# Optimization experiments

Measured on AMD Instinct MI355X. Metric: run time of the kernel, lower is better.

The kernel has to match this reference:

```python
import jax, jax.numpy as jnp
import numpy as np

B, T_OBS, K_PRED, D, U = 1024, 100, 20, 256, 256
T = T_OBS + K_PRED  # len(time_steps) = T_obs + len(time_pred)


def setup_inputs() -> dict:
    key = jax.random.key(0)
    ks = jax.random.split(key, 7)
    latents = jax.random.normal(ks[0], (B, T_OBS, D), dtype=jnp.float32)
    time_steps = jnp.linspace(0.0, 1.0, T, dtype=jnp.float32)
    time_pred = time_steps[-K_PRED:]  # prediction horizon = last K times
    s1 = 1.0 / np.sqrt(D)
    s2 = 1.0 / np.sqrt(U)
    W1 = jax.random.uniform(ks[1], (D, U), jnp.float32, -s1, s1)
    b1 = jax.random.uniform(ks[2], (U,), jnp.float32, -s1, s1)
    W2 = jax.random.uniform(ks[3], (U, U), jnp.float32, -s2, s2)
    b2 = jax.random.uniform(ks[4], (U,), jnp.float32, -s2, s2)
    W3 = jax.random.uniform(ks[5], (U, D), jnp.float32, -s2, s2)
    b3 = jax.random.uniform(ks[6], (D,), jnp.float32, -s2, s2)
    return dict(latents=latents, time_steps=time_steps, time_pred=time_pred,
                W1=W1, b1=b1, W2=W2, b2=b2, W3=W3, b3=b3)


def reference(latents, time_steps, time_pred, W1, b1, W2, b2, W3, b3):
    # ODE-func MLP: latent_dim -> units -> units -> latent_dim (tanh)
    def ode_f(y):
        h = jnp.tanh(y @ W1 + b1)
        h = jnp.tanh(h @ W2 + b2)
        return h @ W3 + b3

    latents_t = jnp.swapaxes(latents, 0, 1)  # [T_obs, B, D]

    # Replicates the original loop semantics exactly: at iteration i the cell
    # integrates from the (prev_t, t_i) left over from iteration i-1 (single
    # Euler step, since every gap < minimum_step = span/50), THEN updates
    # prev_t = t_i, t_i = time_steps[i], and checks membership in time_pred.
    def step(carry, t_next):
        prev_t, t_i, prev_y, j = carry
        yi = prev_y + ode_f(prev_y) * (t_i - prev_t)  # ODECell Euler step
        is_pred = jnp.any(t_next == time_pred)
        j_safe = jnp.clip(j, 0, T_OBS - 1)
        lat_j = jax.lax.dynamic_index_in_dim(latents_t, j_safe, axis=0, keepdims=False)
        prev_y_new = jnp.where(is_pred, yi, lat_j)
        j_new = j + jnp.where(is_pred, 0, 1)
        return (t_i, t_next, prev_y_new, j_new), yi  # Train setting stores yi_ode

    init = (time_steps[0], time_steps[1], latents[:, 0, :], jnp.int32(1))
    _, ys = jax.lax.scan(step, init, time_steps[1:])  # ys: [T-1, B, D]

    new_latents = jnp.concatenate([latents[:, :1, :], jnp.swapaxes(ys, 0, 1)], axis=1)
    return new_latents  # [B, T, D]
```

## Files before the change

### kernel.cpp

```cpp
#include <hip/hip_runtime.h>
#include <hip/hip_bf16.h>

#define NB 1024
#define NTOBS 100
#define NT 120
#define ND 256
#define LAT_BSTRIDE (NTOBS * ND)
#define OUT_BSTRIDE (NT * ND)

#define SEQ_NBLK 64
#define PAR_ROWS 128
#define PAR_BLKS (98 * (NB / PAR_ROWS))

typedef __attribute__((ext_vector_type(8))) short bf16x8;
typedef __attribute__((ext_vector_type(4))) float f32x4;
typedef __attribute__((ext_vector_type(4))) unsigned u32x4;

__device__ __forceinline__ short f2bf(float f) {
    unsigned u = __float_as_uint(f);
    unsigned r = (u + 0x7fffu + ((u >> 16) & 1u)) >> 16;
    return (short)r;
}

__device__ __forceinline__ unsigned cvt_pk_bf16(float lo, float hi) {
    unsigned r;
    asm("v_cvt_pk_bf16_f32 %0, %1, %2" : "=v"(r) : "v"(lo), "v"(hi));
    return r;
}

__device__ __forceinline__ float pade_tanh(float x) {
    float t = fminf(fmaxf(x, -3.0f), 3.0f);
    float t2 = t * t;
    float num = t * (27.0f + t2);
    float den = __builtin_fmaf(9.0f, t2, 27.0f);
    return num * __builtin_amdgcn_rcpf(den);
}

__device__ __forceinline__ int yswz(int r, int c) {
    return (r * 1024 + c * 4) ^ ((r & 7) << 5);
}
__device__ __forceinline__ int aswz(int r, int c) {
    return (r * 512 + c * 2) ^ ((r & 7) << 4);
}

__global__ void prep_kernel(const float* __restrict__ W1,
                            const float* __restrict__ W2,
                            const float* __restrict__ W3,
                            const float* __restrict__ lat,
                            short* __restrict__ wt,
                            float* __restrict__ out)
{
    int tid = blockIdx.x * blockDim.x + threadIdx.x;
    int nth = gridDim.x * blockDim.x;
    for (int i = tid; i < 65536; i += nth) {
        const int j    = i & 7;
        const int lane = (i >> 3) & 63;
        const int kk   = (i >> 9) & 7;
        const int ct16 = i >> 12;
        const int k = kk * 32 + (lane >> 4) * 8 + j;
        const int n = ct16 * 16 + (lane & 15);
        wt[i]              = f2bf(W1[k * 256 + n]);
        wt[i + 65536]      = f2bf(W2[k * 256 + n]);
        wt[i + 2 * 65536]  = f2bf(W3[k * 256 + n]);
    }
    for (int i = tid; i < NB * ND; i += nth) {
        int b = i >> 8, c = i & 255;
        out[(size_t)b * OUT_BSTRIDE + 0 * ND + c] = lat[(size_t)b * LAT_BSTRIDE + 0 * ND + c];
        out[(size_t)b * OUT_BSTRIDE + 2 * ND + c] = lat[(size_t)b * LAT_BSTRIDE + 1 * ND + c];
    }
}

__device__ __forceinline__ void par_layer(f32x4 (&acc)[4][4],
    const char* __restrict__ srcbuf, const short* __restrict__ wtl,
    int rg, int cg, int lane, int l16, int lgr)
{
#pragma unroll
    for (int rt = 0; rt < 4; rt++)
#pragma unroll
        for (int ct = 0; ct < 4; ct++)
            acc[rt][ct] = (f32x4){0.f, 0.f, 0.f, 0.f};

    bf16x8 bpf[4][4];
#pragma unroll
    for (int kk = 0; kk < 4; kk++) {
#pragma unroll
        for (int ct = 0; ct < 4; ct++)
            bpf[kk][ct] = *(const bf16x8*)(wtl + ((cg * 4 + ct) * 8 + kk) * 512 + lane * 8);
    }

#pragma unroll
    for (int kk = 0; kk < 8; kk++) {
        const int k0 = kk * 32 + lgr * 8;
        bf16x8 b[4];
#pragma unroll
        for (int ct = 0; ct < 4; ct++) b[ct] = bpf[kk & 3][ct];
        if (kk < 4) {
#pragma unroll
            for (int ct = 0; ct < 4; ct++)
                bpf[kk][ct] = *(const bf16x8*)(wtl + ((cg * 4 + ct) * 8 + (kk + 4)) * 512 + lane * 8);
        }
        bf16x8 a[4];
#pragma unroll
        for (int rt = 0; rt < 4; rt++) {
            const int r = rg * 64 + rt * 16 + l16;
            a[rt] = *(const bf16x8*)(srcbuf + aswz(r, k0));
        }
#pragma unroll
        for (int rt = 0; rt < 4; rt++)
#pragma unroll
            for (int ct = 0; ct < 4; ct++)
                acc[rt][ct] = __builtin_amdgcn_mfma_f32_16x16x32_bf16(a[rt], b[ct], acc[rt][ct], 0, 0, 0);
    }
}

__device__ __forceinline__ void par_store_h(char* __restrict__ dst,
    const f32x4 (&acc)[4][4], const float bc[4], int rg, int cg, int l16, int lgr)
{
#pragma unroll
    for (int rt = 0; rt < 4; rt++)
#pragma unroll
        for (int ct = 0; ct < 4; ct++) {
            const int c = cg * 64 + ct * 16 + l16;
#pragma unroll
            for (int j = 0; j < 4; j++) {
                const int r = rg * 64 + rt * 16 + lgr * 4 + j;
                *(short*)(dst + aswz(r, c)) = f2bf(pade_tanh(acc[rt][ct][j] + bc[ct]));
            }
        }
}

__global__ __launch_bounds__(512, 2) void ode_main(
    const float* __restrict__ lat, const float* __restrict__ ts,
    const short* __restrict__ wt,
    const float* __restrict__ b1, const float* __restrict__ b2,
    const float* __restrict__ b3, float* __restrict__ out)
{
    __shared__ __align__(16) char smem[131072];

    const int tid = threadIdx.x;
    const int lane = tid & 63, wave = tid >> 6;
    const int l16 = lane & 15, lgr = lane >> 4;
    const short* wt1 = wt;
    const short* wt2 = wt + 65536;
    const short* wt3 = wt + 2 * 65536;

    if (blockIdx.x < SEQ_NBLK) {
        const int b0 = blockIdx.x * 16;
        char* s_y  = smem;
        char* s_h1 = smem + 16384;
        char* s_h2 = smem + 24576;

        bf16x8 w1r[2][8], w2r[2][8], w3r[2][8];
        float bb1[2], bb2[2], bb3[2];
#pragma unroll
        for (int ct = 0; ct < 2; ct++) {
            const int col = wave * 32 + ct * 16 + l16;
            bb1[ct] = b1[col]; bb2[ct] = b2[col]; bb3[ct] = b3[col];
#pragma unroll
            for (int kk = 0; kk < 8; kk++) {
                const int fo = ((wave * 2 + ct) * 8 + kk) * 512 + lane * 8;
                w1r[ct][kk] = *(const bf16x8*)(wt1 + fo);
                w2r[ct][kk] = *(const bf16x8*)(wt2 + fo);
                w3r[ct][kk] = *(const bf16x8*)(wt3 + fo);
            }
        }
        for (int i = tid; i < 16 * 256 / 4; i += 512) {
            const int r = i >> 6, c = (i & 63) * 4;
            f32x4 v = *(const f32x4*)(lat + (size_t)(b0 + r) * LAT_BSTRIDE + 99 * ND + c);
            *(f32x4*)(smem + yswz(r, c)) = v;
        }
        __syncthreads();

#pragma unroll 1
        for (int step = 0; step < 20; step++) {
            const int k = 100 + step;
            const float dt = ts[k - 1] - ts[k - 2];
            f32x4 acc0, acc1;

            acc0 = (f32x4){0.f, 0.f, 0.f, 0.f};
            acc1 = (f32x4){0.f, 0.f, 0.f, 0.f};
#pragma unroll
            for (int kk = 0; kk < 8; kk++) {
                const int k0 = kk * 32 + lgr * 8;
                f32x4 lo = *(const f32x4*)(s_y + yswz(l16, k0));
                f32x4 hi = *(const f32x4*)(s_y + yswz(l16, k0 + 4));
                u32x4 p;
                p[0] = cvt_pk_bf16(lo[0], lo[1]);
                p[1] = cvt_pk_bf16(lo[2], lo[3]);
                p[2] = cvt_pk_bf16(hi[0], hi[1]);
                p[3] = cvt_pk_bf16(hi[2], hi[3]);
                bf16x8 a = *(bf16x8*)&p;
                acc0 = __builtin_amdgcn_mfma_f32_16x16x32_bf16(a, w1r[0][kk], acc0, 0, 0, 0);
                acc1 = __builtin_amdgcn_mfma_f32_16x16x32_bf16(a, w1r[1][kk], acc1, 0, 0, 0);
            }
#pragma unroll
            for (int ct = 0; ct < 2; ct++) {
                const f32x4 av = ct ? acc1 : acc0;
                const int c = wave * 32 + ct * 16 + l16;
#pragma unroll
                for (int j = 0; j < 4; j++) {
                    const int r = lgr * 4 + j;
                    *(short*)(s_h1 + aswz(r, c)) = f2bf(pade_tanh(av[j] + bb1[ct]));
                }
            }
            __syncthreads();

            acc0 = (f32x4){0.f, 0.f, 0.f, 0.f};
            acc1 = (f32x4){0.f, 0.f, 0.f, 0.f};
#pragma unroll
            for (int kk = 0; kk < 8; kk++) {
                const int k0 = kk * 32 + lgr * 8;
                bf16x8 a = *(const bf16x8*)(s_h1 + aswz(l16, k0));
                acc0 = __builtin_amdgcn_mfma_f32_16x16x32_bf16(a, w2r[0][kk], acc0, 0, 0, 0);
                acc1 = __builtin_amdgcn_mfma_f32_16x16x32_bf16(a, w2r[1][kk], acc1, 0, 0, 0);
            }
#pragma unroll
            for (int ct = 0; ct < 2; ct++) {
                const f32x4 av = ct ? acc1 : acc0;
                const int c = wave * 32 + ct * 16 + l16;
#pragma unroll
                for (int j = 0; j < 4; j++) {
                    const int r = lgr * 4 + j;
                    *(short*)(s_h2 + aswz(r, c)) = f2bf(pade_tanh(av[j] + bb2[ct]));
                }
            }
            __syncthreads();

            acc0 = (f32x4){0.f, 0.f, 0.f, 0.f};
            acc1 = (f32x4){0.f, 0.f, 0.f, 0.f};
#pragma unroll
            for (int kk = 0; kk < 8; kk++) {
                const int k0 = kk * 32 + lgr * 8;
                bf16x8 a = *(const bf16x8*)(s_h2 + aswz(l16, k0));
                acc0 = __builtin_amdgcn_mfma_f32_16x16x32_bf16(a, w3r[0][kk], acc0, 0, 0, 0);
                acc1 = __builtin_amdgcn_mfma_f32_16x16x32_bf16(a, w3r[1][kk], acc1, 0, 0, 0);
            }
#pragma unroll
            for (int ct = 0; ct < 2; ct++) {
                const f32x4 av = ct ? acc1 : acc0;
                const int c = wave * 32 + ct * 16 + l16;
                const float bc = ct ? bb3[1] : bb3[0];
#pragma unroll
                for (int j = 0; j < 4; j++) {
                    const int r = lgr * 4 + j;
                    const int yoff = yswz(r, c);
                    const float yold = *(const float*)(s_y + yoff);
                    const float ynew = yold + (av[j] + bc) * dt;
                    *(float*)(s_y + yoff) = ynew;
                    out[(size_t)(b0 + r) * OUT_BSTRIDE + (size_t)k * ND + c] = ynew;
                }
            }
            __syncthreads();
        }
    } else {
        const int p = blockIdx.x - SEQ_NBLK;
        const int e = p >> 3;
        const int b0 = (p & 7) * PAR_ROWS;
        const int src_t = (e == 0) ? 0 : (e + 1);
        const int out_k = (e == 0) ? 1 : (e + 2);
        const float dt = ts[e + 1] - ts[e];
        const float* src = lat + (size_t)b0 * LAT_BSTRIDE + (size_t)src_t * ND;

        char* bufA = smem;
        char* bufH = smem + 65536;
        const int rg = wave >> 2, cg = wave & 3;

#pragma unroll
        for (int t = 0; t < 8; t++) {
            const int i = t * 512 + tid;
            const int r = i >> 5, c0 = (i & 31) * 8;
            const float* pp = src + (size_t)r * LAT_BSTRIDE + c0;
            f32x4 lo = *(const f32x4*)(pp);
            f32x4 hi = *(const f32x4*)(pp + 4);
            u32x4 pk;
            pk[0] = cvt_pk_bf16(lo[0], lo[1]);
            pk[1] = cvt_pk_bf16(lo[2], lo[3]);
            pk[2] = cvt_pk_bf16(hi[0], hi[1]);
            pk[3] = cvt_pk_bf16(hi[2], hi[3]);
            *(u32x4*)(bufA + aswz(r, c0)) = pk;
        }
        __syncthreads();

        f32x4 acc[4][4];
        float bc[4];

#pragma unroll
        for (int ct = 0; ct < 4; ct++) bc[ct] = b1[cg * 64 + ct * 16 + l16];
        par_layer(acc, bufA, wt1, rg, cg, lane, l16, lgr);
        par_store_h(bufH, acc, bc, rg, cg, l16, lgr);
        __syncthreads();

#pragma unroll
        for (int ct = 0; ct < 4; ct++) bc[ct] = b2[cg * 64 + ct * 16 + l16];
        par_layer(acc, bufH, wt2, rg, cg, lane, l16, lgr);
        par_store_h(bufA, acc, bc, rg, cg, l16, lgr);
        __syncthreads();

#pragma unroll
        for (int ct = 0; ct < 4; ct++) bc[ct] = b3[cg * 64 + ct * 16 + l16];
        par_layer(acc, bufA, wt3, rg, cg, lane, l16, lgr);
#pragma unroll
        for (int rt = 0; rt < 4; rt++)
#pragma unroll
            for (int ct = 0; ct < 4; ct++) {
                const int c = cg * 64 + ct * 16 + l16;
#pragma unroll
                for (int j = 0; j < 4; j++) {
                    const int r = rg * 64 + rt * 16 + lgr * 4 + j;
                    const float yold = src[(size_t)r * LAT_BSTRIDE + c];
                    out[(size_t)(b0 + r) * OUT_BSTRIDE + (size_t)out_k * ND + c] =
                        yold + (acc[rt][ct][j] + bc[ct]) * dt;
                }
            }
    }
}

extern "C" void kernel_launch(void* const* d_in, const int* in_sizes, int n_in,
                              void* d_out, int out_size, void* d_ws, size_t ws_size,
                              hipStream_t stream)
{
    const float* lat = (const float*)d_in[0];
    const float* ts  = (const float*)d_in[1];
    const float* W1  = (const float*)d_in[3];
    const float* b1  = (const float*)d_in[4];
    const float* W2  = (const float*)d_in[5];
    const float* b2  = (const float*)d_in[6];
    const float* W3  = (const float*)d_in[7];
    const float* b3  = (const float*)d_in[8];
    float* out = (float*)d_out;
    short* wt = (short*)d_ws;

    hipLaunchKernelGGL(prep_kernel, dim3(256), dim3(256), 0, stream,
                       W1, W2, W3, lat, wt, out);
    hipLaunchKernelGGL(ode_main, dim3(SEQ_NBLK + PAR_BLKS), dim3(512), 0, stream,
                       lat, ts, wt, b1, b2, b3, out);
}
```

Measured before the change: 126.4 us.

## Make parallel MLP blocks persistent with async prefetch of next latent tile

Replaces the 784 one-shot parallel blocks with 192 persistent blocks that each process eight 64-row tiles, prefetching the next tile's fp32 latents into LDS with global_load_lds while the current tile computes. The leftover tiles go to the sequential-recurrence blocks after their 20 steps. Latents now stay fp32 in LDS and are converted to bf16 per MFMA operand, and all 8 K-slices of weights are held in registers. This is meant to hide global load latency and launch/tail cost, at the price of more register pressure, smaller tiles with more weight reloads, and extra work on the sequential blocks.

```diff
diff --git a/kernel.cpp b/kernel.cpp
--- a/kernel.cpp
+++ b/kernel.cpp
@@ -9,8 +9,9 @@
 #define OUT_BSTRIDE (NT * ND)
 
 #define SEQ_NBLK 64
-#define PAR_ROWS 128
-#define PAR_BLKS (98 * (NB / PAR_ROWS))
+#define PAR_PERS 192
+#define NTILES 1568
+#define TILES_PER_BLK 8
 
 typedef __attribute__((ext_vector_type(8))) short bf16x8;
 typedef __attribute__((ext_vector_type(4))) float f32x4;
@@ -41,6 +42,15 @@
 }
 __device__ __forceinline__ int aswz(int r, int c) {
     return (r * 512 + c * 2) ^ ((r & 7) << 4);
+}
+__device__ __forceinline__ int pswz(int r, int c) {
+    return (r * 1024 + c * 4) ^ ((r & 15) << 4);
+}
+
+__device__ __forceinline__ void gload16(const void* g, void* l) {
+    __builtin_amdgcn_global_load_lds(
+        (const __attribute__((address_space(1))) void*)g,
+        (__attribute__((address_space(3))) void*)l, 16, 0, 0);
 }
 
 __global__ void prep_kernel(const float* __restrict__ W1,
@@ -70,61 +80,165 @@
     }
 }
 
-__device__ __forceinline__ void par_layer(f32x4 (&acc)[4][4],
-    const char* __restrict__ srcbuf, const short* __restrict__ wtl,
-    int rg, int cg, int lane, int l16, int lgr)
+__device__ __forceinline__ void stage_issue(const float* __restrict__ lat,
+                                            int t, char* __restrict__ Af32,
+                                            int wave, int lane)
 {
-#pragma unroll
-    for (int rt = 0; rt < 4; rt++)
+    const int e = t >> 4;
+    const int b0 = (t & 15) * 64;
+    const int src_t = (e == 0) ? 0 : (e + 1);
+#pragma unroll
+    for (int i = 0; i < 8; i++) {
+        const int r = i * 8 + wave;
+        const char* src = (const char*)(lat + (size_t)(b0 + r) * LAT_BSTRIDE + (size_t)src_t * ND);
+        gload16(src + ((lane * 16) ^ ((r & 15) << 4)), Af32 + r * 1024);
+    }
+}
+
+__device__ __forceinline__ void par_tile(int t, int tn,
+    const float* __restrict__ lat, const float* __restrict__ ts,
+    const short* __restrict__ wt,
+    const float* __restrict__ b1, const float* __restrict__ b2,
+    const float* __restrict__ b3, float* __restrict__ out,
+    char* __restrict__ Af32, char* __restrict__ hbuf,
+    int wave, int lane, int l16, int lgr)
+{
+    const int e = t >> 4;
+    const int b0 = (t & 15) * 64;
+    const int src_t = (e == 0) ? 0 : (e + 1);
+    const int out_k = (e == 0) ? 1 : (e + 2);
+    const float dt = ts[e + 1] - ts[e];
+    const int rg = wave >> 2, cg = wave & 3;
+    const short* wt1 = wt;
+    const short* wt2 = wt + 65536;
+    const short* wt3 = wt + 2 * 65536;
+
+    f32x4 acc[2][4];
+    bf16x8 ball[8][4];
+    float bc[4];
+
+#pragma unroll
+    for (int kk = 0; kk < 8; kk++)
 #pragma unroll
         for (int ct = 0; ct < 4; ct++)
-            acc[rt][ct] = (f32x4){0.f, 0.f, 0.f, 0.f};
-
-    bf16x8 bpf[4][4];
-#pragma unroll
-    for (int kk = 0; kk < 4; kk++) {
-#pragma unroll
-        for (int ct = 0; ct < 4; ct++)
-            bpf[kk][ct] = *(const bf16x8*)(wtl + ((cg * 4 + ct) * 8 + kk) * 512 + lane * 8);
-    }
-
+            ball[kk][ct] = *(const bf16x8*)(wt1 + ((cg * 4 + ct) * 8 + kk) * 512 + lane * 8);
+#pragma unroll
+    for (int ct = 0; ct < 4; ct++) bc[ct] = b1[cg * 64 + ct * 16 + l16];
+#pragma unroll
+    for (int rt = 0; rt < 2; rt++)
+#pragma unroll
+        for (int ct = 0; ct < 4; ct++) acc[rt][ct] = (f32x4){0.f, 0.f, 0.f, 0.f};
 #pragma unroll
     for (int kk = 0; kk < 8; kk++) {
         const int k0 = kk * 32 + lgr * 8;
-        bf16x8 b[4];
-#pragma unroll
-        for (int ct = 0; ct < 4; ct++) b[ct] = bpf[kk & 3][ct];
-        if (kk < 4) {
+        bf16x8 a[2];
+#pragma unroll
+        for (int rt = 0; rt < 2; rt++) {
+            const int r = rg * 32 + rt * 16 + l16;
+            f32x4 lo = *(const f32x4*)(Af32 + pswz(r, k0));
+            f32x4 hi = *(const f32x4*)(Af32 + pswz(r, k0 + 4));
+            u32x4 p;
+            p[0] = cvt_pk_bf16(lo[0], lo[1]);
+            p[1] = cvt_pk_bf16(lo[2], lo[3]);
+            p[2] = cvt_pk_bf16(hi[0], hi[1]);
+            p[3] = cvt_pk_bf16(hi[2], hi[3]);
+            a[rt] = *(bf16x8*)&p;
+        }
+#pragma unroll
+        for (int rt = 0; rt < 2; rt++)
 #pragma unroll
             for (int ct = 0; ct < 4; ct++)
-                bpf[kk][ct] = *(const bf16x8*)(wtl + ((cg * 4 + ct) * 8 + (kk + 4)) * 512 + lane * 8);
-        }
-        bf16x8 a[4];
-#pragma unroll
-        for (int rt = 0; rt < 4; rt++) {
-            const int r = rg * 64 + rt * 16 + l16;
-            a[rt] = *(const bf16x8*)(srcbuf + aswz(r, k0));
-        }
-#pragma unroll
-        for (int rt = 0; rt < 4; rt++)
-#pragma unroll
-            for (int ct = 0; ct < 4; ct++)
-                acc[rt][ct] = __builtin_amdgcn_mfma_f32_16x16x32_bf16(a[rt], b[ct], acc[rt][ct], 0, 0, 0);
-    }
-}
-
-__device__ __forceinline__ void par_store_h(char* __restrict__ dst,
-    const f32x4 (&acc)[4][4], const float bc[4], int rg, int cg, int l16, int lgr)
-{
-#pragma unroll
-    for (int rt = 0; rt < 4; rt++)
+                acc[rt][ct] = __builtin_amdgcn_mfma_f32_16x16x32_bf16(a[rt], ball[kk][ct], acc[rt][ct], 0, 0, 0);
+    }
+#pragma unroll
+    for (int rt = 0; rt < 2; rt++)
 #pragma unroll
         for (int ct = 0; ct < 4; ct++) {
             const int c = cg * 64 + ct * 16 + l16;
 #pragma unroll
             for (int j = 0; j < 4; j++) {
-                const int r = rg * 64 + rt * 16 + lgr * 4 + j;
-                *(short*)(dst + aswz(r, c)) = f2bf(pade_tanh(acc[rt][ct][j] + bc[ct]));
+                const int r = rg * 32 + rt * 16 + lgr * 4 + j;
+                *(short*)(hbuf + aswz(r, c)) = f2bf(pade_tanh(acc[rt][ct][j] + bc[ct]));
+            }
+        }
+    __syncthreads();
+
+    if (tn >= 0) stage_issue(lat, tn, Af32, wave, lane);
+
+#pragma unroll
+    for (int kk = 0; kk < 8; kk++)
+#pragma unroll
+        for (int ct = 0; ct < 4; ct++)
+            ball[kk][ct] = *(const bf16x8*)(wt2 + ((cg * 4 + ct) * 8 + kk) * 512 + lane * 8);
+#pragma unroll
+    for (int ct = 0; ct < 4; ct++) bc[ct] = b2[cg * 64 + ct * 16 + l16];
+#pragma unroll
+    for (int rt = 0; rt < 2; rt++)
+#pragma unroll
+        for (int ct = 0; ct < 4; ct++) acc[rt][ct] = (f32x4){0.f, 0.f, 0.f, 0.f};
+#pragma unroll
+    for (int kk = 0; kk < 8; kk++) {
+        const int k0 = kk * 32 + lgr * 8;
+        bf16x8 a[2];
+#pragma unroll
+        for (int rt = 0; rt < 2; rt++)
+            a[rt] = *(const bf16x8*)(hbuf + aswz(rg * 32 + rt * 16 + l16, k0));
+#pragma unroll
+        for (int rt = 0; rt < 2; rt++)
+#pragma unroll
+            for (int ct = 0; ct < 4; ct++)
+                acc[rt][ct] = __builtin_amdgcn_mfma_f32_16x16x32_bf16(a[rt], ball[kk][ct], acc[rt][ct], 0, 0, 0);
+    }
+    __syncthreads();
+#pragma unroll
+    for (int rt = 0; rt < 2; rt++)
+#pragma unroll
+        for (int ct = 0; ct < 4; ct++) {
+            const int c = cg * 64 + ct * 16 + l16;
+#pragma unroll
+            for (int j = 0; j < 4; j++) {
+                const int r = rg * 32 + rt * 16 + lgr * 4 + j;
+                *(short*)(hbuf + aswz(r, c)) = f2bf(pade_tanh(acc[rt][ct][j] + bc[ct]));
+            }
+        }
+    __syncthreads();
+
+#pragma unroll
+    for (int kk = 0; kk < 8; kk++)
+#pragma unroll
+        for (int ct = 0; ct < 4; ct++)
+            ball[kk][ct] = *(const bf16x8*)(wt3 + ((cg * 4 + ct) * 8 + kk) * 512 + lane * 8);
+#pragma unroll
+    for (int ct = 0; ct < 4; ct++) bc[ct] = b3[cg * 64 + ct * 16 + l16];
+#pragma unroll
+    for (int rt = 0; rt < 2; rt++)
+#pragma unroll
+        for (int ct = 0; ct < 4; ct++) acc[rt][ct] = (f32x4){0.f, 0.f, 0.f, 0.f};
+#pragma unroll
+    for (int kk = 0; kk < 8; kk++) {
+        const int k0 = kk * 32 + lgr * 8;
+        bf16x8 a[2];
+#pragma unroll
+        for (int rt = 0; rt < 2; rt++)
+            a[rt] = *(const bf16x8*)(hbuf + aswz(rg * 32 + rt * 16 + l16, k0));
+#pragma unroll
+        for (int rt = 0; rt < 2; rt++)
+#pragma unroll
+            for (int ct = 0; ct < 4; ct++)
+                acc[rt][ct] = __builtin_amdgcn_mfma_f32_16x16x32_bf16(a[rt], ball[kk][ct], acc[rt][ct], 0, 0, 0);
+    }
+    const float* src = lat + (size_t)b0 * LAT_BSTRIDE + (size_t)src_t * ND;
+#pragma unroll
+    for (int rt = 0; rt < 2; rt++)
+#pragma unroll
+        for (int ct = 0; ct < 4; ct++) {
+            const int c = cg * 64 + ct * 16 + l16;
+#pragma unroll
+            for (int j = 0; j < 4; j++) {
+                const int r = rg * 32 + rt * 16 + lgr * 4 + j;
+                const float yold = src[(size_t)r * LAT_BSTRIDE + c];
+                out[(size_t)(b0 + r) * OUT_BSTRIDE + (size_t)out_k * ND + c] =
+                    yold + (acc[rt][ct][j] + bc[ct]) * dt;
             }
         }
 }
@@ -135,20 +249,23 @@
     const float* __restrict__ b1, const float* __restrict__ b2,
     const float* __restrict__ b3, float* __restrict__ out)
 {
-    __shared__ __align__(16) char smem[131072];
+    __shared__ __align__(16) char smem[98304];
+    char* Af32 = smem;
+    char* hbuf = smem + 65536;
 
     const int tid = threadIdx.x;
     const int lane = tid & 63, wave = tid >> 6;
     const int l16 = lane & 15, lgr = lane >> 4;
-    const short* wt1 = wt;
-    const short* wt2 = wt + 65536;
-    const short* wt3 = wt + 2 * 65536;
-
-    if (blockIdx.x < SEQ_NBLK) {
-        const int b0 = blockIdx.x * 16;
+    const int bid = blockIdx.x;
+
+    if (bid < SEQ_NBLK) {
+        const int b0 = bid * 16;
         char* s_y  = smem;
         char* s_h1 = smem + 16384;
         char* s_h2 = smem + 24576;
+        const short* wt1 = wt;
+        const short* wt2 = wt + 65536;
+        const short* wt3 = wt + 2 * 65536;
 
         bf16x8 w1r[2][8], w2r[2][8], w3r[2][8];
         float bb1[2], bb2[2], bb3[2];
@@ -167,7 +284,7 @@
         for (int i = tid; i < 16 * 256 / 4; i += 512) {
             const int r = i >> 6, c = (i & 63) * 4;
             f32x4 v = *(const f32x4*)(lat + (size_t)(b0 + r) * LAT_BSTRIDE + 99 * ND + c);
-            *(f32x4*)(smem + yswz(r, c)) = v;
+            *(f32x4*)(s_y + yswz(r, c)) = v;
         }
         __syncthreads();
 
@@ -198,10 +315,8 @@
                 const f32x4 av = ct ? acc1 : acc0;
                 const int c = wave * 32 + ct * 16 + l16;
 #pragma unroll
-                for (int j = 0; j < 4; j++) {
-                    const int r = lgr * 4 + j;
-                    *(short*)(s_h1 + aswz(r, c)) = f2bf(pade_tanh(av[j] + bb1[ct]));
-                }
+                for (int j = 0; j < 4; j++)
+                    *(short*)(s_h1 + aswz(lgr * 4 + j, c)) = f2bf(pade_tanh(av[j] + bb1[ct]));
             }
             __syncthreads();
 
@@ -219,10 +334,8 @@
                 const f32x4 av = ct ? acc1 : acc0;
                 const int c = wave * 32 + ct * 16 + l16;
 #pragma unroll
-                for (int j = 0; j < 4; j++) {
-                    const int r = lgr * 4 + j;
-                    *(short*)(s_h2 + aswz(r, c)) = f2bf(pade_tanh(av[j] + bb2[ct]));
-                }
+                for (int j = 0; j < 4; j++)
+                    *(short*)(s_h2 + aswz(lgr * 4 + j, c)) = f2bf(pade_tanh(av[j] + bb2[ct]));
             }
             __syncthreads();
 
@@ -239,79 +352,38 @@
             for (int ct = 0; ct < 2; ct++) {
                 const f32x4 av = ct ? acc1 : acc0;
                 const int c = wave * 32 + ct * 16 + l16;
-                const float bc = ct ? bb3[1] : bb3[0];
+                const float bcv = ct ? bb3[1] : bb3[0];
 #pragma unroll
                 for (int j = 0; j < 4; j++) {
                     const int r = lgr * 4 + j;
                     const int yoff = yswz(r, c);
                     const float yold = *(const float*)(s_y + yoff);
-                    const float ynew = yold + (av[j] + bc) * dt;
+                    const float ynew = yold + (av[j] + bcv) * dt;
                     *(float*)(s_y + yoff) = ynew;
                     out[(size_t)(b0 + r) * OUT_BSTRIDE + (size_t)k * ND + c] = ynew;
                 }
             }
             __syncthreads();
         }
+
+        if (bid < NTILES - PAR_PERS * TILES_PER_BLK) {
+            const int t = PAR_PERS * TILES_PER_BLK + bid;
+            stage_issue(lat, t, Af32, wave, lane);
+            __syncthreads();
+            par_tile(t, -1, lat, ts, wt, b1, b2, b3, out, Af32, hbuf,
+                     wave, lane, l16, lgr);
+        }
     } else {
-        const int p = blockIdx.x - SEQ_NBLK;
-        const int e = p >> 3;
-        const int b0 = (p & 7) * PAR_ROWS;
-        const int src_t = (e == 0) ? 0 : (e + 1);
-        const int out_k = (e == 0) ? 1 : (e + 2);
-        const float dt = ts[e + 1] - ts[e];
-        const float* src = lat + (size_t)b0 * LAT_BSTRIDE + (size_t)src_t * ND;
-
-        char* bufA = smem;
-        char* bufH = smem + 65536;
-        const int rg = wave >> 2, cg = wave & 3;
-
-#pragma unroll
-        for (int t = 0; t < 8; t++) {
-            const int i = t * 512 + tid;
-            const int r = i >> 5, c0 = (i & 31) * 8;
-            const float* pp = src + (size_t)r * LAT_BSTRIDE + c0;
-            f32x4 lo = *(const f32x4*)(pp);
-            f32x4 hi = *(const f32x4*)(pp + 4);
-            u32x4 pk;
-            pk[0] = cvt_pk_bf16(lo[0], lo[1]);
-            pk[1] = cvt_pk_bf16(lo[2], lo[3]);
-            pk[2] = cvt_pk_bf16(hi[0], hi[1]);
-            pk[3] = cvt_pk_bf16(hi[2], hi[3]);
-            *(u32x4*)(bufA + aswz(r, c0)) = pk;
-        }
-        __syncthreads();
-
-        f32x4 acc[4][4];
-        float bc[4];
-
-#pragma unroll
-        for (int ct = 0; ct < 4; ct++) bc[ct] = b1[cg * 64 + ct * 16 + l16];
-        par_layer(acc, bufA, wt1, rg, cg, lane, l16, lgr);
-        par_store_h(bufH, acc, bc, rg, cg, l16, lgr);
-        __syncthreads();
-
-#pragma unroll
-        for (int ct = 0; ct < 4; ct++) bc[ct] = b2[cg * 64 + ct * 16 + l16];
-        par_layer(acc, bufH, wt2, rg, cg, lane, l16, lgr);
-        par_store_h(bufA, acc, bc, rg, cg, l16, lgr);
-        __syncthreads();
-
-#pragma unroll
-        for (int ct = 0; ct < 4; ct++) bc[ct] = b3[cg * 64 + ct * 16 + l16];
-        par_layer(acc, bufA, wt3, rg, cg, lane, l16, lgr);
-#pragma unroll
-        for (int rt = 0; rt < 4; rt++)
-#pragma unroll
-            for (int ct = 0; ct < 4; ct++) {
-                const int c = cg * 64 + ct * 16 + l16;
-#pragma unroll
-                for (int j = 0; j < 4; j++) {
-                    const int r = rg * 64 + rt * 16 + lgr * 4 + j;
-                    const float yold = src[(size_t)r * LAT_BSTRIDE + c];
-                    out[(size_t)(b0 + r) * OUT_BSTRIDE + (size_t)out_k * ND + c] =
-                        yold + (acc[rt][ct][j] + bc[ct]) * dt;
-                }
-            }
+        const int first = (bid - SEQ_NBLK) * TILES_PER_BLK;
+        stage_issue(lat, first, Af32, wave, lane);
+#pragma unroll 1
+        for (int n = 0; n < TILES_PER_BLK; n++) {
+            __syncthreads();
+            const int t = first + n;
+            const int tn = (n + 1 < TILES_PER_BLK) ? (t + 1) : -1;
+            par_tile(t, tn, lat, ts, wt, b1, b2, b3, out, Af32, hbuf,
+                     wave, lane, l16, lgr);
+        }
     }
 }
 
@@ -332,6 +404,6 @@
 
     hipLaunchKernelGGL(prep_kernel, dim3(256), dim3(256), 0, stream,
                        W1, W2, W3, lat, wt, out);
-    hipLaunchKernelGGL(ode_main, dim3(SEQ_NBLK + PAR_BLKS), dim3(512), 0, stream,
+    hipLaunchKernelGGL(ode_main, dim3(SEQ_NBLK + PAR_PERS), dim3(512), 0, stream,
                        lat, ts, wt, b1, b2, b3, out);
 }
```

After: 315.5 us. 150% more time.

## Split fused ODE kernel into separate sequential and parallel kernels

Applied to the files above, without the earlier changes.

The single launch that mixed sequential prediction blocks with parallel Euler-step blocks becomes two kernels. The sequential 20-step recurrence gets its own small-LDS kernel. The parallel kernel now uses 256-thread blocks over 64 rows with 64KB of LDS and a looped layer body, which should allow more resident blocks per CU. The trade-off is that both kernels are on the same stream, so the latency-bound sequential part no longer overlaps with the bandwidth-bound parallel part.

```diff
diff --git a/kernel.cpp b/kernel.cpp
--- a/kernel.cpp
+++ b/kernel.cpp
@@ -9,7 +9,7 @@
 #define OUT_BSTRIDE (NT * ND)
 
 #define SEQ_NBLK 64
-#define PAR_ROWS 128
+#define PAR_ROWS 64
 #define PAR_BLKS (98 * (NB / PAR_ROWS))
 
 typedef __attribute__((ext_vector_type(8))) short bf16x8;
@@ -70,249 +70,237 @@
     }
 }
 
-__device__ __forceinline__ void par_layer(f32x4 (&acc)[4][4],
-    const char* __restrict__ srcbuf, const short* __restrict__ wtl,
-    int rg, int cg, int lane, int l16, int lgr)
-{
-#pragma unroll
-    for (int rt = 0; rt < 4; rt++)
-#pragma unroll
-        for (int ct = 0; ct < 4; ct++)
-            acc[rt][ct] = (f32x4){0.f, 0.f, 0.f, 0.f};
-
-    bf16x8 bpf[4][4];
-#pragma unroll
-    for (int kk = 0; kk < 4; kk++) {
-#pragma unroll
-        for (int ct = 0; ct < 4; ct++)
-            bpf[kk][ct] = *(const bf16x8*)(wtl + ((cg * 4 + ct) * 8 + kk) * 512 + lane * 8);
-    }
-
-#pragma unroll
-    for (int kk = 0; kk < 8; kk++) {
-        const int k0 = kk * 32 + lgr * 8;
-        bf16x8 b[4];
-#pragma unroll
-        for (int ct = 0; ct < 4; ct++) b[ct] = bpf[kk & 3][ct];
-        if (kk < 4) {
-#pragma unroll
-            for (int ct = 0; ct < 4; ct++)
-                bpf[kk][ct] = *(const bf16x8*)(wtl + ((cg * 4 + ct) * 8 + (kk + 4)) * 512 + lane * 8);
-        }
-        bf16x8 a[4];
-#pragma unroll
-        for (int rt = 0; rt < 4; rt++) {
-            const int r = rg * 64 + rt * 16 + l16;
-            a[rt] = *(const bf16x8*)(srcbuf + aswz(r, k0));
-        }
-#pragma unroll
-        for (int rt = 0; rt < 4; rt++)
-#pragma unroll
-            for (int ct = 0; ct < 4; ct++)
-                acc[rt][ct] = __builtin_amdgcn_mfma_f32_16x16x32_bf16(a[rt], b[ct], acc[rt][ct], 0, 0, 0);
-    }
-}
-
-__device__ __forceinline__ void par_store_h(char* __restrict__ dst,
-    const f32x4 (&acc)[4][4], const float bc[4], int rg, int cg, int l16, int lgr)
-{
-#pragma unroll
-    for (int rt = 0; rt < 4; rt++)
-#pragma unroll
-        for (int ct = 0; ct < 4; ct++) {
-            const int c = cg * 64 + ct * 16 + l16;
-#pragma unroll
-            for (int j = 0; j < 4; j++) {
-                const int r = rg * 64 + rt * 16 + lgr * 4 + j;
-                *(short*)(dst + aswz(r, c)) = f2bf(pade_tanh(acc[rt][ct][j] + bc[ct]));
-            }
-        }
-}
-
-__global__ __launch_bounds__(512, 2) void ode_main(
+__global__ __launch_bounds__(512, 2) void ode_seq(
     const float* __restrict__ lat, const float* __restrict__ ts,
     const short* __restrict__ wt,
     const float* __restrict__ b1, const float* __restrict__ b2,
     const float* __restrict__ b3, float* __restrict__ out)
 {
-    __shared__ __align__(16) char smem[131072];
+    __shared__ __align__(16) char smem[32768];
+    char* s_y  = smem;
+    char* s_h1 = smem + 16384;
+    char* s_h2 = smem + 24576;
 
     const int tid = threadIdx.x;
     const int lane = tid & 63, wave = tid >> 6;
     const int l16 = lane & 15, lgr = lane >> 4;
+    const int b0 = blockIdx.x * 16;
     const short* wt1 = wt;
     const short* wt2 = wt + 65536;
     const short* wt3 = wt + 2 * 65536;
 
-    if (blockIdx.x < SEQ_NBLK) {
-        const int b0 = blockIdx.x * 16;
-        char* s_y  = smem;
-        char* s_h1 = smem + 16384;
-        char* s_h2 = smem + 24576;
-
-        bf16x8 w1r[2][8], w2r[2][8], w3r[2][8];
-        float bb1[2], bb2[2], bb3[2];
+    bf16x8 w1r[2][8], w2r[2][8], w3r[2][8];
+    float bb1[2], bb2[2], bb3[2];
+#pragma unroll
+    for (int ct = 0; ct < 2; ct++) {
+        const int col = wave * 32 + ct * 16 + l16;
+        bb1[ct] = b1[col]; bb2[ct] = b2[col]; bb3[ct] = b3[col];
+#pragma unroll
+        for (int kk = 0; kk < 8; kk++) {
+            const int fo = ((wave * 2 + ct) * 8 + kk) * 512 + lane * 8;
+            w1r[ct][kk] = *(const bf16x8*)(wt1 + fo);
+            w2r[ct][kk] = *(const bf16x8*)(wt2 + fo);
+            w3r[ct][kk] = *(const bf16x8*)(wt3 + fo);
+        }
+    }
+    for (int i = tid; i < 16 * 256 / 4; i += 512) {
+        const int r = i >> 6, c = (i & 63) * 4;
+        f32x4 v = *(const f32x4*)(lat + (size_t)(b0 + r) * LAT_BSTRIDE + 99 * ND + c);
+        *(f32x4*)(s_y + yswz(r, c)) = v;
+    }
+    __syncthreads();
+
+#pragma unroll 1
+    for (int step = 0; step < 20; step++) {
+        const int k = 100 + step;
+        const float dt = ts[k - 1] - ts[k - 2];
+        f32x4 acc0, acc1;
+
+        acc0 = (f32x4){0.f, 0.f, 0.f, 0.f};
+        acc1 = (f32x4){0.f, 0.f, 0.f, 0.f};
+#pragma unroll
+        for (int kk = 0; kk < 8; kk++) {
+            const int k0 = kk * 32 + lgr * 8;
+            f32x4 lo = *(const f32x4*)(s_y + yswz(l16, k0));
+            f32x4 hi = *(const f32x4*)(s_y + yswz(l16, k0 + 4));
+            u32x4 p;
+            p[0] = cvt_pk_bf16(lo[0], lo[1]);
+            p[1] = cvt_pk_bf16(lo[2], lo[3]);
+            p[2] = cvt_pk_bf16(hi[0], hi[1]);
+            p[3] = cvt_pk_bf16(hi[2], hi[3]);
+            bf16x8 a = *(bf16x8*)&p;
+            acc0 = __builtin_amdgcn_mfma_f32_16x16x32_bf16(a, w1r[0][kk], acc0, 0, 0, 0);
+            acc1 = __builtin_amdgcn_mfma_f32_16x16x32_bf16(a, w1r[1][kk], acc1, 0, 0, 0);
+        }
 #pragma unroll
         for (int ct = 0; ct < 2; ct++) {
-            const int col = wave * 32 + ct * 16 + l16;
-            bb1[ct] = b1[col]; bb2[ct] = b2[col]; bb3[ct] = b3[col];
-#pragma unroll
-            for (int kk = 0; kk < 8; kk++) {
-                const int fo = ((wave * 2 + ct) * 8 + kk) * 512 + lane * 8;
-                w1r[ct][kk] = *(const bf16x8*)(wt1 + fo);
-                w2r[ct][kk] = *(const bf16x8*)(wt2 + fo);
-                w3r[ct][kk] = *(const bf16x8*)(wt3 + fo);
+            const f32x4 av = ct ? acc1 : acc0;
+            const int c = wave * 32 + ct * 16 + l16;
+#pragma unroll
+            for (int j = 0; j < 4; j++)
+                *(short*)(s_h1 + aswz(lgr * 4 + j, c)) = f2bf(pade_tanh(av[j] + bb1[ct]));
+        }
+        __syncthreads();
+
+        acc0 = (f32x4){0.f, 0.f, 0.f, 0.f};
+        acc1 = (f32x4){0.f, 0.f, 0.f, 0.f};
+#pragma unroll
+        for (int kk = 0; kk < 8; kk++) {
+            const int k0 = kk * 32 + lgr * 8;
+            bf16x8 a = *(const bf16x8*)(s_h1 + aswz(l16, k0));
+            acc0 = __builtin_amdgcn_mfma_f32_16x16x32_bf16(a, w2r[0][kk], acc0, 0, 0, 0);
+            acc1 = __builtin_amdgcn_mfma_f32_16x16x32_bf16(a, w2r[1][kk], acc1, 0, 0, 0);
+        }
+#pragma unroll
+        for (int ct = 0; ct < 2; ct++) {
+            const f32x4 av = ct ? acc1 : acc0;
+            const int c = wave * 32 + ct * 16 + l16;
+#pragma unroll
+            for (int j = 0; j < 4; j++)
+                *(short*)(s_h2 + aswz(lgr * 4 + j, c)) = f2bf(pade_tanh(av[j] + bb2[ct]));
+        }
+        __syncthreads();
+
+        acc0 = (f32x4){0.f, 0.f, 0.f, 0.f};
+        acc1 = (f32x4){0.f, 0.f, 0.f, 0.f};
+#pragma unroll
+        for (int kk = 0; kk < 8; kk++) {
+            const int k0 = kk * 32 + lgr * 8;
+            bf16x8 a = *(const bf16x8*)(s_h2 + aswz(l16, k0));
+            acc0 = __builtin_amdgcn_mfma_f32_16x16x32_bf16(a, w3r[0][kk], acc0, 0, 0, 0);
+            acc1 = __builtin_amdgcn_mfma_f32_16x16x32_bf16(a, w3r[1][kk], acc1, 0, 0, 0);
+        }
+#pragma unroll
+        for (int ct = 0; ct < 2; ct++) {
+            const f32x4 av = ct ? acc1 : acc0;
+            const int c = wave * 32 + ct * 16 + l16;
+            const float bcv = ct ? bb3[1] : bb3[0];
+#pragma unroll
+            for (int j = 0; j < 4; j++) {
+                const int r = lgr * 4 + j;
+                const int yoff = yswz(r, c);
+                const float yold = *(const float*)(s_y + yoff);
+                const float ynew = yold + (av[j] + bcv) * dt;
+                *(float*)(s_y + yoff) = ynew;
+                out[(size_t)(b0 + r) * OUT_BSTRIDE + (size_t)k * ND + c] = ynew;
             }
         }
-        for (int i = tid; i < 16 * 256 / 4; i += 512) {
-            const int r = i >> 6, c = (i & 63) * 4;
-            f32x4 v = *(const f32x4*)(lat + (size_t)(b0 + r) * LAT_BSTRIDE + 99 * ND + c);
-            *(f32x4*)(smem + yswz(r, c)) = v;
-        }
         __syncthreads();
+    }
+}
+
+__global__ __launch_bounds__(256, 2) void ode_par(
+    const float* __restrict__ lat, const float* __restrict__ ts,
+    const short* __restrict__ wt,
+    const float* __restrict__ b1, const float* __restrict__ b2,
+    const float* __restrict__ b3, float* __restrict__ out)
+{
+    __shared__ __align__(16) char smem[65536];
+    char* bufA = smem;
+    char* bufH = smem + 32768;
+
+    const int tid = threadIdx.x;
+    const int lane = tid & 63, cg = tid >> 6;
+    const int l16 = lane & 15, lgr = lane >> 4;
+    const int p = blockIdx.x;
+    const int e = p >> 4;
+    const int b0 = (p & 15) * PAR_ROWS;
+    const int src_t = (e == 0) ? 0 : (e + 1);
+    const int out_k = (e == 0) ? 1 : (e + 2);
+    const float dt = ts[e + 1] - ts[e];
+    const float* src = lat + (size_t)b0 * LAT_BSTRIDE + (size_t)src_t * ND;
+    const short* wtl[3] = { wt, wt + 65536, wt + 2 * 65536 };
+
+#pragma unroll
+    for (int t = 0; t < 8; t++) {
+        const int i = t * 256 + tid;
+        const int r = i >> 5, c0 = (i & 31) * 8;
+        const float* pp = src + (size_t)r * LAT_BSTRIDE + c0;
+        f32x4 lo = *(const f32x4*)(pp);
+        f32x4 hi = *(const f32x4*)(pp + 4);
+        u32x4 pk;
+        pk[0] = cvt_pk_bf16(lo[0], lo[1]);
+        pk[1] = cvt_pk_bf16(lo[2], lo[3]);
+        pk[2] = cvt_pk_bf16(hi[0], hi[1]);
+        pk[3] = cvt_pk_bf16(hi[2], hi[3]);
+        *(u32x4*)(bufA + aswz(r, c0)) = pk;
+    }
+    __syncthreads();
+
+    f32x4 acc[4][4];
+    float bc[4];
 
 #pragma unroll 1
-        for (int step = 0; step < 20; step++) {
-            const int k = 100 + step;
-            const float dt = ts[k - 1] - ts[k - 2];
-            f32x4 acc0, acc1;
-
-            acc0 = (f32x4){0.f, 0.f, 0.f, 0.f};
-            acc1 = (f32x4){0.f, 0.f, 0.f, 0.f};
-#pragma unroll
-            for (int kk = 0; kk < 8; kk++) {
-                const int k0 = kk * 32 + lgr * 8;
-                f32x4 lo = *(const f32x4*)(s_y + yswz(l16, k0));
-                f32x4 hi = *(const f32x4*)(s_y + yswz(l16, k0 + 4));
-                u32x4 p;
-                p[0] = cvt_pk_bf16(lo[0], lo[1]);
-                p[1] = cvt_pk_bf16(lo[2], lo[3]);
-                p[2] = cvt_pk_bf16(hi[0], hi[1]);
-                p[3] = cvt_pk_bf16(hi[2], hi[3]);
-                bf16x8 a = *(bf16x8*)&p;
-                acc0 = __builtin_amdgcn_mfma_f32_16x16x32_bf16(a, w1r[0][kk], acc0, 0, 0, 0);
-                acc1 = __builtin_amdgcn_mfma_f32_16x16x32_bf16(a, w1r[1][kk], acc1, 0, 0, 0);
+    for (int layer = 0; layer < 3; layer++) {
+        const char* sbuf = (layer == 1) ? bufH : bufA;
+        char* dbuf = (layer == 1) ? bufA : bufH;
+        const short* wl = wtl[layer];
+        const float* bias = (layer == 0) ? b1 : (layer == 1) ? b2 : b3;
+#pragma unroll
+        for (int ct = 0; ct < 4; ct++) bc[ct] = bias[cg * 64 + ct * 16 + l16];
+#pragma unroll
+        for (int rt = 0; rt < 4; rt++)
+#pragma unroll
+            for (int ct = 0; ct < 4; ct++) acc[rt][ct] = (f32x4){0.f, 0.f, 0.f, 0.f};
+
+        bf16x8 bpf[4][4];
+#pragma unroll
+        for (int kk = 0; kk < 4; kk++)
+#pragma unroll
+            for (int ct = 0; ct < 4; ct++)
+                bpf[kk][ct] = *(const bf16x8*)(wl + ((cg * 4 + ct) * 8 + kk) * 512 + lane * 8);
+
+#pragma unroll
+        for (int kk = 0; kk < 8; kk++) {
+            const int k0 = kk * 32 + lgr * 8;
+            bf16x8 b[4];
+#pragma unroll
+            for (int ct = 0; ct < 4; ct++) b[ct] = bpf[kk & 3][ct];
+            if (kk < 4) {
+#pragma unroll
+                for (int ct = 0; ct < 4; ct++)
+                    bpf[kk][ct] = *(const bf16x8*)(wl + ((cg * 4 + ct) * 8 + (kk + 4)) * 512 + lane * 8);
             }
-#pragma unroll
-            for (int ct = 0; ct < 2; ct++) {
-                const f32x4 av = ct ? acc1 : acc0;
-                const int c = wave * 32 + ct * 16 + l16;
-#pragma unroll
-                for (int j = 0; j < 4; j++) {
-                    const int r = lgr * 4 + j;
-                    *(short*)(s_h1 + aswz(r, c)) = f2bf(pade_tanh(av[j] + bb1[ct]));
+            bf16x8 a[4];
+#pragma unroll
+            for (int rt = 0; rt < 4; rt++)
+                a[rt] = *(const bf16x8*)(sbuf + aswz(rt * 16 + l16, k0));
+#pragma unroll
+            for (int rt = 0; rt < 4; rt++)
+#pragma unroll
+                for (int ct = 0; ct < 4; ct++)
+                    acc[rt][ct] = __builtin_amdgcn_mfma_f32_16x16x32_bf16(a[rt], b[ct], acc[rt][ct], 0, 0, 0);
+        }
+
+        if (layer < 2) {
+#pragma unroll
+            for (int rt = 0; rt < 4; rt++)
+#pragma unroll
+                for (int ct = 0; ct < 4; ct++) {
+                    const int c = cg * 64 + ct * 16 + l16;
+#pragma unroll
+                    for (int j = 0; j < 4; j++) {
+                        const int r = rt * 16 + lgr * 4 + j;
+                        *(short*)(dbuf + aswz(r, c)) = f2bf(pade_tanh(acc[rt][ct][j] + bc[ct]));
+                    }
                 }
+            __syncthreads();
+        }
+    }
+
+#pragma unroll
+    for (int rt = 0; rt < 4; rt++)
+#pragma unroll
+        for (int ct = 0; ct < 4; ct++) {
+            const int c = cg * 64 + ct * 16 + l16;
+#pragma unroll
+            for (int j = 0; j < 4; j++) {
+                const int r = rt * 16 + lgr * 4 + j;
+                const float yold = src[(size_t)r * LAT_BSTRIDE + c];
+                out[(size_t)(b0 + r) * OUT_BSTRIDE + (size_t)out_k * ND + c] =
+                    yold + (acc[rt][ct][j] + bc[ct]) * dt;
             }
-            __syncthreads();
-
-            acc0 = (f32x4){0.f, 0.f, 0.f, 0.f};
-            acc1 = (f32x4){0.f, 0.f, 0.f, 0.f};
-#pragma unroll
-            for (int kk = 0; kk < 8; kk++) {
-                const int k0 = kk * 32 + lgr * 8;
-                bf16x8 a = *(const bf16x8*)(s_h1 + aswz(l16, k0));
-                acc0 = __builtin_amdgcn_mfma_f32_16x16x32_bf16(a, w2r[0][kk], acc0, 0, 0, 0);
-                acc1 = __builtin_amdgcn_mfma_f32_16x16x32_bf16(a, w2r[1][kk], acc1, 0, 0, 0);
-            }
-#pragma unroll
-            for (int ct = 0; ct < 2; ct++) {
-                const f32x4 av = ct ? acc1 : acc0;
-                const int c = wave * 32 + ct * 16 + l16;
-#pragma unroll
-                for (int j = 0; j < 4; j++) {
-                    const int r = lgr * 4 + j;
-                    *(short*)(s_h2 + aswz(r, c)) = f2bf(pade_tanh(av[j] + bb2[ct]));
-                }
-            }
-            __syncthreads();
-
-            acc0 = (f32x4){0.f, 0.f, 0.f, 0.f};
-            acc1 = (f32x4){0.f, 0.f, 0.f, 0.f};
-#pragma unroll
-            for (int kk = 0; kk < 8; kk++) {
-                const int k0 = kk * 32 + lgr * 8;
-                bf16x8 a = *(const bf16x8*)(s_h2 + aswz(l16, k0));
-                acc0 = __builtin_amdgcn_mfma_f32_16x16x32_bf16(a, w3r[0][kk], acc0, 0, 0, 0);
-                acc1 = __builtin_amdgcn_mfma_f32_16x16x32_bf16(a, w3r[1][kk], acc1, 0, 0, 0);
-            }
-#pragma unroll
-            for (int ct = 0; ct < 2; ct++) {
-                const f32x4 av = ct ? acc1 : acc0;
-                const int c = wave * 32 + ct * 16 + l16;
-                const float bc = ct ? bb3[1] : bb3[0];
-#pragma unroll
-                for (int j = 0; j < 4; j++) {
-                    const int r = lgr * 4 + j;
-                    const int yoff = yswz(r, c);
-                    const float yold = *(const float*)(s_y + yoff);
-                    const float ynew = yold + (av[j] + bc) * dt;
-                    *(float*)(s_y + yoff) = ynew;
-                    out[(size_t)(b0 + r) * OUT_BSTRIDE + (size_t)k * ND + c] = ynew;
-                }
-            }
-            __syncthreads();
-        }
-    } else {
-        const int p = blockIdx.x - SEQ_NBLK;
-        const int e = p >> 3;
-        const int b0 = (p & 7) * PAR_ROWS;
-        const int src_t = (e == 0) ? 0 : (e + 1);
-        const int out_k = (e == 0) ? 1 : (e + 2);
-        const float dt = ts[e + 1] - ts[e];
-        const float* src = lat + (size_t)b0 * LAT_BSTRIDE + (size_t)src_t * ND;
-
-        char* bufA = smem;
-        char* bufH = smem + 65536;
-        const int rg = wave >> 2, cg = wave & 3;
-
-#pragma unroll
-        for (int t = 0; t < 8; t++) {
-            const int i = t * 512 + tid;
-            const int r = i >> 5, c0 = (i & 31) * 8;
-            const float* pp = src + (size_t)r * LAT_BSTRIDE + c0;
-            f32x4 lo = *(const f32x4*)(pp);
-            f32x4 hi = *(const f32x4*)(pp + 4);
-            u32x4 pk;
-            pk[0] = cvt_pk_bf16(lo[0], lo[1]);
-            pk[1] = cvt_pk_bf16(lo[2], lo[3]);
-            pk[2] = cvt_pk_bf16(hi[0], hi[1]);
-            pk[3] = cvt_pk_bf16(hi[2], hi[3]);
-            *(u32x4*)(bufA + aswz(r, c0)) = pk;
-        }
-        __syncthreads();
-
-        f32x4 acc[4][4];
-        float bc[4];
-
-#pragma unroll
-        for (int ct = 0; ct < 4; ct++) bc[ct] = b1[cg * 64 + ct * 16 + l16];
-        par_layer(acc, bufA, wt1, rg, cg, lane, l16, lgr);
-        par_store_h(bufH, acc, bc, rg, cg, l16, lgr);
-        __syncthreads();
-
-#pragma unroll
-        for (int ct = 0; ct < 4; ct++) bc[ct] = b2[cg * 64 + ct * 16 + l16];
-        par_layer(acc, bufH, wt2, rg, cg, lane, l16, lgr);
-        par_store_h(bufA, acc, bc, rg, cg, l16, lgr);
-        __syncthreads();
-
-#pragma unroll
-        for (int ct = 0; ct < 4; ct++) bc[ct] = b3[cg * 64 + ct * 16 + l16];
-        par_layer(acc, bufA, wt3, rg, cg, lane, l16, lgr);
-#pragma unroll
-        for (int rt = 0; rt < 4; rt++)
-#pragma unroll
-            for (int ct = 0; ct < 4; ct++) {
-                const int c = cg * 64 + ct * 16 + l16;
-#pragma unroll
-                for (int j = 0; j < 4; j++) {
-                    const int r = rg * 64 + rt * 16 + lgr * 4 + j;
-                    const float yold = src[(size_t)r * LAT_BSTRIDE + c];
-                    out[(size_t)(b0 + r) * OUT_BSTRIDE + (size_t)out_k * ND + c] =
-                        yold + (acc[rt][ct][j] + bc[ct]) * dt;
-                }
-            }
-    }
+        }
 }
 
 extern "C" void kernel_launch(void* const* d_in, const int* in_sizes, int n_in,
@@ -332,6 +320,8 @@
 
     hipLaunchKernelGGL(prep_kernel, dim3(256), dim3(256), 0, stream,
                        W1, W2, W3, lat, wt, out);
-    hipLaunchKernelGGL(ode_main, dim3(SEQ_NBLK + PAR_BLKS), dim3(512), 0, stream,
+    hipLaunchKernelGGL(ode_seq, dim3(SEQ_NBLK), dim3(512), 0, stream,
                        lat, ts, wt, b1, b2, b3, out);
-}
+    hipLaunchKernelGGL(ode_par, dim3(PAR_BLKS), dim3(256), 0, stream,
+                       lat, ts, wt, b1, b2, b3, out);
+}
```

Result: slower. 161.2 us (+27.5%).
